# Performance work log

Hardware: AMD Instinct MI355X
Metric: run time of the kernel (lower is better)

Reference implementation:

```python
import jax, jax.numpy as jnp
import numpy as np

DIM = 512
HEADS = 16
WIN = (7, 7)
N = WIN[0] * WIN[1]
B_ = 4096
HEAD_DIM = DIM // HEADS
SCALE = HEAD_DIM ** (-0.5)


def _relative_position_index():
    ch = np.arange(WIN[0])
    cw = np.arange(WIN[1])
    coords = np.stack(np.meshgrid(ch, cw, indexing='ij'))  # (2, Wh, Ww)
    cf = coords.reshape(2, -1)                               # (2, N)
    rel = cf[:, :, None] - cf[:, None, :]                    # (2, N, N)
    rel = rel.transpose(1, 2, 0).astype(np.int32)            # (N, N, 2)
    rel[:, :, 0] += WIN[0] - 1
    rel[:, :, 1] += WIN[1] - 1
    rel[:, :, 0] *= 2 * WIN[1] - 1
    return jnp.asarray(rel.sum(-1))                          # (N, N) int32


def setup_inputs() -> dict:
    key = jax.random.key(0)
    ks = jax.random.split(key, 6)
    x = jax.random.normal(ks[0], (B_, N, DIM), dtype=jnp.float32)
    qkv_w = jax.random.normal(ks[1], (3 * DIM, DIM), dtype=jnp.float32) * (DIM ** -0.5)
    qkv_b = jnp.zeros((3 * DIM,), dtype=jnp.float32)
    proj_w = jax.random.normal(ks[2], (DIM, DIM), dtype=jnp.float32) * (DIM ** -0.5)
    proj_b = jnp.zeros((DIM,), dtype=jnp.float32)
    n_rel = (2 * WIN[0] - 1) * (2 * WIN[1] - 1)  # 169
    bias_table = jax.random.normal(ks[3], (n_rel, HEADS), dtype=jnp.float32) * 0.02
    rel_idx = _relative_position_index()
    return {"x": x, "qkv_w": qkv_w, "qkv_b": qkv_b, "proj_w": proj_w,
            "proj_b": proj_b, "bias_table": bias_table, "rel_idx": rel_idx}


def reference(x, qkv_w, qkv_b, proj_w, proj_b, bias_table, rel_idx):
    B, n, C = x.shape
    # qkv projection: (B, N, 3C) -> (3, B, H, N, hd)
    qkv = x @ qkv_w.T + qkv_b
    qkv = qkv.reshape(B, n, 3, HEADS, HEAD_DIM).transpose(2, 0, 3, 1, 4)
    q, k, v = qkv[0], qkv[1], qkv[2]
    q = q * SCALE
    attn = jnp.einsum('bhnd,bhmd->bhnm', q, k)               # (B, H, N, N)
    # gather relative position bias: (N*N, H) -> (H, N, N)
    bias = bias_table[rel_idx.reshape(-1)].reshape(n, n, HEADS).transpose(2, 0, 1)
    attn = jax.nn.softmax(attn + bias[None], axis=-1)
    out = jnp.einsum('bhnm,bhmd->bhnd', attn, v)
    out = out.transpose(0, 2, 1, 3).reshape(B, n, C)
    return out @ proj_w.T + proj_b
```

## Files before the change

kernel.cpp:

```cpp
#include <hip/hip_runtime.h>
#include <cstdint>
#include <type_traits>

#define B_WIN 4096
#define NTOK 49
#define DIMC 512
#define HEADS 16
#define HD 32
#define M_ROWS (B_WIN * NTOK)
#define SCALE 0.17677669529663689f

using bf16x8 = __attribute__((ext_vector_type(8))) short;
using f32x4  = __attribute__((ext_vector_type(4))) float;
using u16x8  = __attribute__((ext_vector_type(8))) unsigned short;

__device__ inline unsigned short f2bf(float f) {
    uint32_t u = __float_as_uint(f);
    uint32_t r = (u + 0x7fffu + ((u >> 16) & 1u)) >> 16;
    return (unsigned short)r;
}
__device__ inline unsigned int pk2(float lo, float hi) {
    return (unsigned int)f2bf(lo) | ((unsigned int)f2bf(hi) << 16);
}

__global__ __launch_bounds__(256) void cvt_f32_bf16(
    const float* __restrict__ in, unsigned short* __restrict__ out, int n4)
{
    for (int i = blockIdx.x * blockDim.x + threadIdx.x; i < n4;
         i += gridDim.x * blockDim.x) {
        float4 v = reinterpret_cast<const float4*>(in)[i];
        ushort4 o;
        o.x = f2bf(v.x); o.y = f2bf(v.y); o.z = f2bf(v.z); o.w = f2bf(v.w);
        reinterpret_cast<ushort4*>(out)[i] = o;
    }
}

__global__ __launch_bounds__(256) void build_bias(
    const float* __restrict__ btab, const int* __restrict__ ridx,
    float* __restrict__ biasPad)
{
    const int idx = blockIdx.x * 256 + threadIdx.x;
    const int h = idx >> 12, rem = idx & 4095;
    const int i = rem >> 6, j = rem & 63;
    float v = -1e30f;
    if (i < NTOK && j < NTOK) v = btab[ridx[i * NTOK + j] * HEADS + h];
    biasPad[idx] = v;
}

template <int A_F32, int OUT_F32>
__global__ __launch_bounds__(256) void gemm_bf16(
    const void* __restrict__ Araw,
    const unsigned short* __restrict__ W,
    const float* __restrict__ bias,
    void* __restrict__ Craw,
    int M, int N, int K, int ntn)
{
    __shared__ unsigned short As[128 * 32];
    __shared__ unsigned short Bs[128 * 32];

    const int nwg = gridDim.x;
    const int bid = blockIdx.x;
    const int wg = (bid & 7) * (nwg >> 3) + (bid >> 3);
    const int tn = wg % ntn, tm = wg / ntn;
    const size_t m0 = (size_t)tm * 128, n0 = (size_t)tn * 128;

    const int t = threadIdx.x;
    const int lane = t & 63;
    const int l15 = lane & 15, l4 = lane >> 4;
    const int wrow = (t >> 7) * 64;
    const int wcol = ((t >> 6) & 1) * 64;

    f32x4 acc[4][4] = {};

    for (int kt = 0; kt < K; kt += 32) {
#pragma unroll
        for (int i = 0; i < 2; ++i) {
            const int f = i * 256 + t;
            const int row = f >> 2;
            const int kq = (f & 3) << 3;
            const unsigned short* gb = W + (n0 + row) * K + kt + kq;
            __builtin_amdgcn_global_load_lds(
                (const __attribute__((address_space(1))) void*)gb,
                (__attribute__((address_space(3))) void*)(Bs + f * 8), 16, 0, 0);
        }
        if constexpr (A_F32) {
            const float* A = (const float*)Araw;
#pragma unroll
            for (int i = 0; i < 2; ++i) {
                const int f = i * 256 + t;
                const int row = f >> 2;
                const int kq = (f & 3) << 3;
                const float* ga = A + (m0 + row) * K + kt + kq;
                const float4 a0 = *reinterpret_cast<const float4*>(ga);
                const float4 a1 = *reinterpret_cast<const float4*>(ga + 4);
                u16x8 pk;
                pk[0] = f2bf(a0.x); pk[1] = f2bf(a0.y);
                pk[2] = f2bf(a0.z); pk[3] = f2bf(a0.w);
                pk[4] = f2bf(a1.x); pk[5] = f2bf(a1.y);
                pk[6] = f2bf(a1.z); pk[7] = f2bf(a1.w);
                *reinterpret_cast<u16x8*>(As + f * 8) = pk;
            }
        } else {
            const unsigned short* A = (const unsigned short*)Araw;
#pragma unroll
            for (int i = 0; i < 2; ++i) {
                const int f = i * 256 + t;
                const int row = f >> 2;
                const int kq = (f & 3) << 3;
                const unsigned short* ga = A + (m0 + row) * K + kt + kq;
                __builtin_amdgcn_global_load_lds(
                    (const __attribute__((address_space(1))) void*)ga,
                    (__attribute__((address_space(3))) void*)(As + f * 8), 16, 0, 0);
            }
        }
        __syncthreads();

        bf16x8 a[4], b[4];
#pragma unroll
        for (int m = 0; m < 4; ++m)
            a[m] = *(const bf16x8*)(As + (wrow + m * 16 + l15) * 32 + l4 * 8);
#pragma unroll
        for (int n = 0; n < 4; ++n)
            b[n] = *(const bf16x8*)(Bs + (wcol + n * 16 + l15) * 32 + l4 * 8);
#pragma unroll
        for (int m = 0; m < 4; ++m)
#pragma unroll
            for (int n = 0; n < 4; ++n)
                acc[m][n] = __builtin_amdgcn_mfma_f32_16x16x32_bf16(
                    a[m], b[n], acc[m][n], 0, 0, 0);
        __syncthreads();
    }

#pragma unroll
    for (int m = 0; m < 4; ++m) {
#pragma unroll
        for (int n = 0; n < 4; ++n) {
            const size_t col = n0 + wcol + n * 16 + l15;
            const float bv = bias[col];
#pragma unroll
            for (int r = 0; r < 4; ++r) {
                const size_t row = m0 + wrow + m * 16 + l4 * 4 + r;
                const float v = acc[m][n][r] + bv;
                if constexpr (OUT_F32)
                    ((float*)Craw)[row * N + col] = v;
                else
                    ((unsigned short*)Craw)[row * N + col] = f2bf(v);
            }
        }
    }
}

__global__ __launch_bounds__(256) void attn_mfma(
    const unsigned short* __restrict__ qkv,
    const float* __restrict__ biasPad,
    unsigned short* __restrict__ attn_out)
{
    __shared__ unsigned short vtile[4][32][72];

    const int w = threadIdx.x >> 6;
    const int g = blockIdx.x * 4 + w;
    const int b = g >> 4, h = g & 15;
    const int lane = threadIdx.x & 63;
    const int l15 = lane & 15, l4 = lane >> 4;

    bf16x8 aq[4], bk[4], vload[4];
#pragma unroll
    for (int mt = 0; mt < 4; ++mt) {
        const int tok = mt * 16 + l15;
        bf16x8 zq = {}, zk = {}, zv = {};
        if (tok < NTOK) {
            const unsigned short* base =
                qkv + (size_t)(b * NTOK + tok) * 1536 + h * HD + l4 * 8;
            zq = *(const bf16x8*)base;
            zk = *(const bf16x8*)(base + 512);
            zv = *(const bf16x8*)(base + 1024);
        }
        aq[mt] = zq; bk[mt] = zk; vload[mt] = zv;
    }

#pragma unroll
    for (int mt = 0; mt < 4; ++mt) {
        const int tok = mt * 16 + l15;
#pragma unroll
        for (int e = 0; e < 8; ++e)
            vtile[w][l4 * 8 + e][tok] = (unsigned short)vload[mt][e];
    }

    f32x4 sacc[4][4] = {};
#pragma unroll
    for (int nt = 0; nt < 4; ++nt)
#pragma unroll
        for (int mt = 0; mt < 4; ++mt)
            sacc[nt][mt] = __builtin_amdgcn_mfma_f32_16x16x32_bf16(
                bk[nt], aq[mt], sacc[nt][mt], 0, 0, 0);

    const float* bb = biasPad + (h << 12);
    unsigned int pw[4][4][2];
#pragma unroll
    for (int mt = 0; mt < 4; ++mt) {
        const int i = mt * 16 + l15;
        const float* brow = bb + i * 64 + l4 * 4;
        float mx = -3.0e38f;
#pragma unroll
        for (int nt = 0; nt < 4; ++nt) {
            const float4 b4 = *(const float4*)(brow + nt * 16);
            const float v0 = fmaf(sacc[nt][mt][0], SCALE, b4.x);
            const float v1 = fmaf(sacc[nt][mt][1], SCALE, b4.y);
            const float v2 = fmaf(sacc[nt][mt][2], SCALE, b4.z);
            const float v3 = fmaf(sacc[nt][mt][3], SCALE, b4.w);
            sacc[nt][mt][0] = v0; sacc[nt][mt][1] = v1;
            sacc[nt][mt][2] = v2; sacc[nt][mt][3] = v3;
            mx = fmaxf(mx, fmaxf(fmaxf(v0, v1), fmaxf(v2, v3)));
        }
        mx = fmaxf(mx, __shfl_xor(mx, 16));
        mx = fmaxf(mx, __shfl_xor(mx, 32));
        float sum = 0.f;
#pragma unroll
        for (int nt = 0; nt < 4; ++nt) {
            const float e0 = __expf(sacc[nt][mt][0] - mx);
            const float e1 = __expf(sacc[nt][mt][1] - mx);
            const float e2 = __expf(sacc[nt][mt][2] - mx);
            const float e3 = __expf(sacc[nt][mt][3] - mx);
            sacc[nt][mt][0] = e0; sacc[nt][mt][1] = e1;
            sacc[nt][mt][2] = e2; sacc[nt][mt][3] = e3;
            sum += (e0 + e1) + (e2 + e3);
        }
        sum += __shfl_xor(sum, 16);
        sum += __shfl_xor(sum, 32);
        const float inv = 1.0f / sum;
#pragma unroll
        for (int nt = 0; nt < 4; ++nt) {
            pw[mt][nt][0] = pk2(sacc[nt][mt][0] * inv, sacc[nt][mt][1] * inv);
            pw[mt][nt][1] = pk2(sacc[nt][mt][2] * inv, sacc[nt][mt][3] * inv);
        }
    }

    bf16x8 ap[4][2];
#pragma unroll
    for (int mt = 0; mt < 4; ++mt)
#pragma unroll
        for (int ks = 0; ks < 2; ++ks) {
            union { int wv[4]; bf16x8 v; } u;
#pragma unroll
            for (int q = 0; q < 4; ++q) {
                const int src = l15 + ((2 * (l4 & 1) + (q >> 1)) << 4);
                const int va = __shfl((int)pw[mt][2 * ks][q & 1], src);
                const int vb = __shfl((int)pw[mt][2 * ks + 1][q & 1], src);
                u.wv[q] = (l4 & 2) ? vb : va;
            }
            ap[mt][ks] = u.v;
        }

    bf16x8 bv2[2][2];
#pragma unroll
    for (int n = 0; n < 2; ++n)
#pragma unroll
        for (int ks = 0; ks < 2; ++ks)
            bv2[n][ks] = *(const bf16x8*)&vtile[w][n * 16 + l15][ks * 32 + l4 * 8];

    f32x4 oacc[4][2] = {};
#pragma unroll
    for (int mt = 0; mt < 4; ++mt)
#pragma unroll
        for (int n = 0; n < 2; ++n)
#pragma unroll
            for (int ks = 0; ks < 2; ++ks)
                oacc[mt][n] = __builtin_amdgcn_mfma_f32_16x16x32_bf16(
                    ap[mt][ks], bv2[n][ks], oacc[mt][n], 0, 0, 0);

#pragma unroll
    for (int mt = 0; mt < 4; ++mt) {
#pragma unroll
        for (int r = 0; r < 4; ++r) {
            const int i = mt * 16 + l4 * 4 + r;
            if (i < NTOK) {
                unsigned short* op =
                    attn_out + (size_t)(b * NTOK + i) * DIMC + h * HD + l15;
                op[0]  = f2bf(oacc[mt][0][r]);
                op[16] = f2bf(oacc[mt][1][r]);
            }
        }
    }
}

extern "C" void kernel_launch(void* const* d_in, const int* in_sizes, int n_in,
                              void* d_out, int out_size, void* d_ws, size_t ws_size,
                              hipStream_t stream)
{
    const float* x      = (const float*)d_in[0];
    const float* qkv_w  = (const float*)d_in[1];
    const float* qkv_b  = (const float*)d_in[2];
    const float* proj_w = (const float*)d_in[3];
    const float* proj_b = (const float*)d_in[4];
    const float* btab   = (const float*)d_in[5];
    const int*   ridx   = (const int*)d_in[6];
    float* out = (float*)d_out;

    char* w = (char*)d_ws;
    const size_t SZ_QKVW  = (size_t)1536 * 512 * 2;
    const size_t SZ_PROJW = (size_t)512 * 512 * 2;
    const size_t SZ_BIAS  = (size_t)HEADS * 64 * 64 * 4;
    const size_t SZ_QKV   = (size_t)M_ROWS * 1536 * 2;
    unsigned short* qkvw_bf  = (unsigned short*)w;
    unsigned short* projw_bf = (unsigned short*)(w + SZ_QKVW);
    float*          biasPad  = (float*)(w + SZ_QKVW + SZ_PROJW);
    unsigned short* qkv      = (unsigned short*)(w + SZ_QKVW + SZ_PROJW + SZ_BIAS);
    unsigned short* attn_out = (unsigned short*)((char*)qkv + SZ_QKV);

    cvt_f32_bf16<<<128, 256, 0, stream>>>(qkv_w, qkvw_bf, 1536 * 512 / 4);
    cvt_f32_bf16<<<64, 256, 0, stream>>>(proj_w, projw_bf, 512 * 512 / 4);
    build_bias<<<256, 256, 0, stream>>>(btab, ridx, biasPad);

    gemm_bf16<1, 0><<<18816, 256, 0, stream>>>(
        x, qkvw_bf, qkv_b, qkv, M_ROWS, 1536, 512, 12);

    attn_mfma<<<16384, 256, 0, stream>>>(qkv, biasPad, attn_out);

    gemm_bf16<0, 1><<<6272, 256, 0, stream>>>(
        attn_out, projw_bf, proj_b, out, M_ROWS, 512, 512, 4);
}
```

Baseline: 1.143 ms.

## Replace GEMMs with 256x256 double-buffered 8-wave pipelined MFMA kernel

Both projection GEMMs are replaced by a 512-thread kernel that computes 256x256 tiles with K-step 64. It uses 128KB of double-buffered LDS with an XOR swizzle, direct global-to-LDS loads interleaved with MFMA phases, and setprio and explicit waitcnt scheduling. The input x is now converted to bf16 in a separate pass so that both operands can use async LDS loads. This adds an extra full read and write of x, and the kernel relies on 128KB of shared memory and hand-tuned barriers.

Result: faster. 938.9 us (-17.9%).

```diff
diff --git a/kernel.cpp b/kernel.cpp
--- a/kernel.cpp
+++ b/kernel.cpp
@@ -22,6 +22,17 @@
 __device__ inline unsigned int pk2(float lo, float hi) {
     return (unsigned int)f2bf(lo) | ((unsigned int)f2bf(hi) << 16);
 }
+
+__device__ __forceinline__ void gll16(const unsigned short* g, unsigned short* l) {
+    __builtin_amdgcn_global_load_lds(
+        (const __attribute__((address_space(1))) void*)g,
+        (__attribute__((address_space(3))) void*)l, 16, 0, 0);
+}
+
+#define DSR(dst, addr) asm volatile("ds_read_b128 %0, %1" : "=v"(dst) : "v"(addr))
+#define SCHED0() __builtin_amdgcn_sched_barrier(0)
+#define BARRIER() do { SCHED0(); __builtin_amdgcn_s_barrier(); SCHED0(); } while (0)
+#define LGKM0() do { asm volatile("s_waitcnt lgkmcnt(0)"); SCHED0(); } while (0)
 
 __global__ __launch_bounds__(256) void cvt_f32_bf16(
     const float* __restrict__ in, unsigned short* __restrict__ out, int n4)
@@ -47,107 +58,167 @@
     biasPad[idx] = v;
 }
 
-template <int A_F32, int OUT_F32>
-__global__ __launch_bounds__(256) void gemm_bf16(
-    const void* __restrict__ Araw,
+template <int OUTF32>
+__global__ __launch_bounds__(512, 2) void gemm8p(
+    const unsigned short* __restrict__ A,
     const unsigned short* __restrict__ W,
     const float* __restrict__ bias,
     void* __restrict__ Craw,
-    int M, int N, int K, int ntn)
+    int N, int ntn)
 {
-    __shared__ unsigned short As[128 * 32];
-    __shared__ unsigned short Bs[128 * 32];
+    extern __shared__ unsigned short lds[];
+    constexpr int K = 512, NT = 8;
 
     const int nwg = gridDim.x;
     const int bid = blockIdx.x;
     const int wg = (bid & 7) * (nwg >> 3) + (bid >> 3);
     const int tn = wg % ntn, tm = wg / ntn;
-    const size_t m0 = (size_t)tm * 128, n0 = (size_t)tn * 128;
+    const size_t m0 = (size_t)tm * 256, n0 = (size_t)tn * 256;
 
     const int t = threadIdx.x;
-    const int lane = t & 63;
+    const int lane = t & 63, wid = t >> 6;
+    const int wm = wid >> 2, wn = wid & 3;
     const int l15 = lane & 15, l4 = lane >> 4;
-    const int wrow = (t >> 7) * 64;
-    const int wcol = ((t >> 6) & 1) * 64;
-
-    f32x4 acc[4][4] = {};
-
-    for (int kt = 0; kt < K; kt += 32) {
-#pragma unroll
-        for (int i = 0; i < 2; ++i) {
-            const int f = i * 256 + t;
-            const int row = f >> 2;
-            const int kq = (f & 3) << 3;
-            const unsigned short* gb = W + (n0 + row) * K + kt + kq;
-            __builtin_amdgcn_global_load_lds(
-                (const __attribute__((address_space(1))) void*)gb,
-                (__attribute__((address_space(3))) void*)(Bs + f * 8), 16, 0, 0);
-        }
-        if constexpr (A_F32) {
-            const float* A = (const float*)Araw;
-#pragma unroll
-            for (int i = 0; i < 2; ++i) {
-                const int f = i * 256 + t;
-                const int row = f >> 2;
-                const int kq = (f & 3) << 3;
-                const float* ga = A + (m0 + row) * K + kt + kq;
-                const float4 a0 = *reinterpret_cast<const float4*>(ga);
-                const float4 a1 = *reinterpret_cast<const float4*>(ga + 4);
-                u16x8 pk;
-                pk[0] = f2bf(a0.x); pk[1] = f2bf(a0.y);
-                pk[2] = f2bf(a0.z); pk[3] = f2bf(a0.w);
-                pk[4] = f2bf(a1.x); pk[5] = f2bf(a1.y);
-                pk[6] = f2bf(a1.z); pk[7] = f2bf(a1.w);
-                *reinterpret_cast<u16x8*>(As + f * 8) = pk;
-            }
-        } else {
-            const unsigned short* A = (const unsigned short*)Araw;
-#pragma unroll
-            for (int i = 0; i < 2; ++i) {
-                const int f = i * 256 + t;
-                const int row = f >> 2;
-                const int kq = (f & 3) << 3;
-                const unsigned short* ga = A + (m0 + row) * K + kt + kq;
-                __builtin_amdgcn_global_load_lds(
-                    (const __attribute__((address_space(1))) void*)ga,
-                    (__attribute__((address_space(3))) void*)(As + f * 8), 16, 0, 0);
-            }
-        }
-        __syncthreads();
-
-        bf16x8 a[4], b[4];
+
+    const unsigned short* pA[2];
+    const unsigned short* pB[2];
+    int dA[2], dB[2];
+#pragma unroll
+    for (int u = 0; u < 2; ++u) {
+        const int f = t + u * 512, rl = f >> 3, c = f & 7, g = c ^ (rl & 7);
+        const int lrA = (rl & 63) + (rl >> 6) * 128;
+        const int lrB = ((rl >> 5) << 6) + (rl & 31);
+        pA[u] = A + (m0 + lrA) * K + g * 8;
+        pB[u] = W + (n0 + lrB) * K + g * 8;
+        dA[u] = lrA * 64 + c * 8;
+        dB[u] = 32768 + lrB * 64 + c * 8;
+    }
+#define STG_A(h, T) { const int _b = ((T) & 1) * 16384, _kt = (T) * 64;      \
+    gll16(pA[0] + (h) * 64 * K + _kt, lds + _b + dA[0] + (h) * 4096);        \
+    gll16(pA[1] + (h) * 64 * K + _kt, lds + _b + dA[1] + (h) * 4096); }
+#define STG_B(h, T) { const int _b = ((T) & 1) * 16384, _kt = (T) * 64;      \
+    gll16(pB[0] + (h) * 32 * K + _kt, lds + _b + dB[0] + (h) * 2048);        \
+    gll16(pB[1] + (h) * 32 * K + _kt, lds + _b + dB[1] + (h) * 2048); }
+
+    const unsigned lbase = (unsigned)(uintptr_t)lds;
+    const unsigned swz = (unsigned)(l15 & 7);
+    const unsigned cx0 = ((0u + l4) ^ swz) * 16u;
+    const unsigned cx1 = ((4u + l4) ^ swz) * 16u;
+    const unsigned arow = (unsigned)(wm * 128 + l15) * 128u;
+    const unsigned brow = (unsigned)(wn * 64 + l15) * 128u;
+
+    f32x4 acc[8][4] = {};
+    bf16x8 a[4][2], b0[2][2], b1[2][2];
+
+    STG_A(0, 0); STG_B(0, 0); STG_A(1, 0); STG_B(1, 0);
+    STG_A(0, 1); STG_B(0, 1); STG_A(1, 1);
+    asm volatile("s_waitcnt vmcnt(6)");
+    SCHED0();
+    BARRIER();
+
+    for (int S = 0; S < NT; ++S) {
+        const int bs = S & 1;
+        const unsigned ab = lbase + (unsigned)bs * 32768u;
+        const unsigned bb = lbase + 65536u + (unsigned)bs * 32768u;
+
+#pragma unroll
+        for (int m = 0; m < 4; ++m) {
+            DSR(a[m][0], ab + arow + m * 2048u + cx0);
+            DSR(a[m][1], ab + arow + m * 2048u + cx1);
+        }
+#pragma unroll
+        for (int n = 0; n < 2; ++n) {
+            DSR(b0[n][0], bb + brow + n * 2048u + cx0);
+            DSR(b0[n][1], bb + brow + n * 2048u + cx1);
+        }
+        if (S + 1 < NT) STG_B(1, S + 1);
+        BARRIER(); LGKM0();
+        __builtin_amdgcn_s_setprio(1);
 #pragma unroll
         for (int m = 0; m < 4; ++m)
-            a[m] = *(const bf16x8*)(As + (wrow + m * 16 + l15) * 32 + l4 * 8);
-#pragma unroll
-        for (int n = 0; n < 4; ++n)
-            b[n] = *(const bf16x8*)(Bs + (wcol + n * 16 + l15) * 32 + l4 * 8);
+#pragma unroll
+            for (int n = 0; n < 2; ++n)
+#pragma unroll
+                for (int ks = 0; ks < 2; ++ks)
+                    acc[m][n] = __builtin_amdgcn_mfma_f32_16x16x32_bf16(
+                        a[m][ks], b0[n][ks], acc[m][n], 0, 0, 0);
+        __builtin_amdgcn_s_setprio(0);
+        BARRIER();
+
+#pragma unroll
+        for (int n = 0; n < 2; ++n) {
+            DSR(b1[n][0], bb + brow + (n + 2) * 2048u + cx0);
+            DSR(b1[n][1], bb + brow + (n + 2) * 2048u + cx1);
+        }
+        if (S + 2 < NT) STG_A(0, S + 2);
+        BARRIER(); LGKM0();
+        __builtin_amdgcn_s_setprio(1);
 #pragma unroll
         for (int m = 0; m < 4; ++m)
 #pragma unroll
-            for (int n = 0; n < 4; ++n)
-                acc[m][n] = __builtin_amdgcn_mfma_f32_16x16x32_bf16(
-                    a[m], b[n], acc[m][n], 0, 0, 0);
-        __syncthreads();
-    }
-
-#pragma unroll
-    for (int m = 0; m < 4; ++m) {
+            for (int n = 0; n < 2; ++n)
+#pragma unroll
+                for (int ks = 0; ks < 2; ++ks)
+                    acc[m][n + 2] = __builtin_amdgcn_mfma_f32_16x16x32_bf16(
+                        a[m][ks], b1[n][ks], acc[m][n + 2], 0, 0, 0);
+        __builtin_amdgcn_s_setprio(0);
+        BARRIER();
+
+#pragma unroll
+        for (int m = 0; m < 4; ++m) {
+            DSR(a[m][0], ab + arow + 8192u + m * 2048u + cx0);
+            DSR(a[m][1], ab + arow + 8192u + m * 2048u + cx1);
+        }
+        if (S + 2 < NT) STG_B(0, S + 2);
+        BARRIER(); LGKM0();
+        __builtin_amdgcn_s_setprio(1);
+#pragma unroll
+        for (int m = 0; m < 4; ++m)
+#pragma unroll
+            for (int n = 0; n < 2; ++n)
+#pragma unroll
+                for (int ks = 0; ks < 2; ++ks)
+                    acc[m + 4][n] = __builtin_amdgcn_mfma_f32_16x16x32_bf16(
+                        a[m][ks], b0[n][ks], acc[m + 4][n], 0, 0, 0);
+        __builtin_amdgcn_s_setprio(0);
+        BARRIER();
+
+        if (S + 2 < NT) STG_A(1, S + 2);
+        if (S < NT - 2)       { asm volatile("s_waitcnt vmcnt(6)"); SCHED0(); }
+        else if (S == NT - 2) { asm volatile("s_waitcnt vmcnt(0)"); SCHED0(); }
+        BARRIER();
+        __builtin_amdgcn_s_setprio(1);
+#pragma unroll
+        for (int m = 0; m < 4; ++m)
+#pragma unroll
+            for (int n = 0; n < 2; ++n)
+#pragma unroll
+                for (int ks = 0; ks < 2; ++ks)
+                    acc[m + 4][n + 2] = __builtin_amdgcn_mfma_f32_16x16x32_bf16(
+                        a[m][ks], b1[n][ks], acc[m + 4][n + 2], 0, 0, 0);
+        __builtin_amdgcn_s_setprio(0);
+        BARRIER();
+    }
+
+#pragma unroll
+    for (int m = 0; m < 8; ++m) {
 #pragma unroll
         for (int n = 0; n < 4; ++n) {
-            const size_t col = n0 + wcol + n * 16 + l15;
+            const size_t col = n0 + wn * 64 + n * 16 + l15;
             const float bv = bias[col];
 #pragma unroll
             for (int r = 0; r < 4; ++r) {
-                const size_t row = m0 + wrow + m * 16 + l4 * 4 + r;
+                const size_t row = m0 + wm * 128 + m * 16 + l4 * 4 + r;
                 const float v = acc[m][n][r] + bv;
-                if constexpr (OUT_F32)
+                if constexpr (OUTF32)
                     ((float*)Craw)[row * N + col] = v;
                 else
                     ((unsigned short*)Craw)[row * N + col] = f2bf(v);
             }
         }
     }
+#undef STG_A
+#undef STG_B
 }
 
 __global__ __launch_bounds__(256) void attn_mfma(
@@ -297,25 +368,33 @@
     float* out = (float*)d_out;
 
     char* w = (char*)d_ws;
+    const size_t SZ_XBF   = (size_t)M_ROWS * DIMC * 2;
     const size_t SZ_QKVW  = (size_t)1536 * 512 * 2;
     const size_t SZ_PROJW = (size_t)512 * 512 * 2;
     const size_t SZ_BIAS  = (size_t)HEADS * 64 * 64 * 4;
     const size_t SZ_QKV   = (size_t)M_ROWS * 1536 * 2;
-    unsigned short* qkvw_bf  = (unsigned short*)w;
-    unsigned short* projw_bf = (unsigned short*)(w + SZ_QKVW);
-    float*          biasPad  = (float*)(w + SZ_QKVW + SZ_PROJW);
-    unsigned short* qkv      = (unsigned short*)(w + SZ_QKVW + SZ_PROJW + SZ_BIAS);
+    unsigned short* x_bf     = (unsigned short*)w;
+    unsigned short* qkvw_bf  = (unsigned short*)(w + SZ_XBF);
+    unsigned short* projw_bf = (unsigned short*)(w + SZ_XBF + SZ_QKVW);
+    float*          biasPad  = (float*)(w + SZ_XBF + SZ_QKVW + SZ_PROJW);
+    unsigned short* qkv      = (unsigned short*)(w + SZ_XBF + SZ_QKVW + SZ_PROJW + SZ_BIAS);
     unsigned short* attn_out = (unsigned short*)((char*)qkv + SZ_QKV);
 
+    hipFuncSetAttribute(reinterpret_cast<const void*>(&gemm8p<0>),
+                        hipFuncAttributeMaxDynamicSharedMemorySize, 131072);
+    hipFuncSetAttribute(reinterpret_cast<const void*>(&gemm8p<1>),
+                        hipFuncAttributeMaxDynamicSharedMemorySize, 131072);
+
+    cvt_f32_bf16<<<2048, 256, 0, stream>>>(x, x_bf, M_ROWS * DIMC / 4);
     cvt_f32_bf16<<<128, 256, 0, stream>>>(qkv_w, qkvw_bf, 1536 * 512 / 4);
     cvt_f32_bf16<<<64, 256, 0, stream>>>(proj_w, projw_bf, 512 * 512 / 4);
     build_bias<<<256, 256, 0, stream>>>(btab, ridx, biasPad);
 
-    gemm_bf16<1, 0><<<18816, 256, 0, stream>>>(
-        x, qkvw_bf, qkv_b, qkv, M_ROWS, 1536, 512, 12);
+    gemm8p<0><<<4704, 512, 131072, stream>>>(
+        x_bf, qkvw_bf, qkv_b, qkv, 1536, 6);
 
     attn_mfma<<<16384, 256, 0, stream>>>(qkv, biasPad, attn_out);
 
-    gemm_bf16<0, 1><<<6272, 256, 0, stream>>>(
-        attn_out, projw_bf, proj_b, out, M_ROWS, 512, 512, 4);
-}
+    gemm8p<1><<<1568, 512, 131072, stream>>>(
+        attn_out, projw_bf, proj_b, out, 512, 2);
+}
```
